# Performance work log

Measured on AMD Instinct MI355X. Metric: run time of the kernel, lower is better.

The kernel has to match this reference:

```python
import jax, jax.numpy as jnp
import numpy as np

D_K = 64
N_STEPS = 4
NEG = -1e9  # stand-in for -inf; keeps vjp NaN-free, numerically identical softmax


def setup_inputs() -> dict:
    key = jax.random.key(0)
    ks = jax.random.split(key, 12)
    B, N, D = 4, 2048, 1024
    s = 0.02
    return {
        "hidden": jax.random.normal(ks[0], (B, N, D), jnp.float32),
        "W1": jax.random.normal(ks[1], (64, D), jnp.float32) * s,
        "b1": jnp.zeros((64,), jnp.float32),
        "W2": jax.random.normal(ks[2], (28, 64), jnp.float32) * s,
        "b2": jnp.zeros((28,), jnp.float32),
        "Wq": jax.random.normal(ks[3], (D_K, 28), jnp.float32) * s,
        "Wk": jax.random.normal(ks[4], (D_K, 28), jnp.float32) * s,
        "Wc": jax.random.normal(ks[5], (1, 28), jnp.float32) * s,
        "bc": jnp.zeros((1,), jnp.float32),
        "Wv": jax.random.normal(ks[6], (D_K, D), jnp.float32) * s,
        "Wo": jax.random.normal(ks[7], (D, D_K), jnp.float32) * s,  # torch inits this to zeros; randomized for a non-trivial baseline
        "step_size": jnp.asarray(0.5, jnp.float32),
        "charge_decay": jnp.asarray(0.3, jnp.float32),
        "layer_idx": 0,
    }


def reference(hidden, W1, b1, W2, b2, Wq, Wk, Wc, bc, Wv, Wo, step_size, charge_decay, layer_idx):
    B, N, D = hidden.shape
    # features come from detached hidden in the torch code
    h_sg = jax.lax.stop_gradient(hidden)
    f = jax.nn.gelu(h_sg @ W1.T + b1, approximate=False)  # [B,N,64]
    features = jax.nn.sigmoid(f @ W2.T + b2)              # [B,N,28]
    Q = features @ Wq.T                                   # [B,N,64]
    K = features @ Wk.T                                   # [B,N,64]
    compat = jnp.einsum('bnd,bmd->bnm', Q, K) / jnp.float32(np.sqrt(D_K))
    charge = jax.nn.sigmoid(features @ Wc.T + bc)[..., 0]  # [B,N]
    causal = jnp.tril(jnp.ones((N, N), dtype=bool))
    logits = jnp.where(causal, compat, NEG)
    for _ in range(N_STEPS):
        attn = jax.nn.softmax(logits, axis=-1)            # [B,N,N]
        received = attn.sum(axis=-2)                      # [B,N]
        charge = charge * (1.0 - charge_decay * jax.nn.sigmoid(received - 1.0))
        energy = -compat * charge[:, :, None] * charge[:, None, :]
        logits = jnp.where(causal, logits - step_size * energy, NEG)
    attn = jax.nn.softmax(logits, axis=-1)
    V = hidden @ Wv.T                                     # [B,N,64]
    out = jnp.einsum('bnm,bmd->bnd', attn, V) @ Wo.T      # [B,N,D]
    return out * 0.1
```

## Files before the change

### kernel.cpp

```cpp
#include <hip/hip_runtime.h>
#include <hip/hip_bf16.h>

typedef unsigned short ushort_t;
typedef short bf16x8 __attribute__((ext_vector_type(8)));
typedef ushort_t u16x8 __attribute__((ext_vector_type(8)));
typedef ushort_t u16x4 __attribute__((ext_vector_type(4)));
typedef float f32x4 __attribute__((ext_vector_type(4)));

#define DEV static __device__ __forceinline__

DEV float bf2f(ushort_t u) { unsigned v = ((unsigned)u) << 16; float f; __builtin_memcpy(&f, &v, 4); return f; }
DEV short f2bf(float x) { __hip_bfloat16 h = __float2bfloat16(x); short s; __builtin_memcpy(&s, &h, 2); return s; }
DEV float sigm(float x) { return 1.0f / (1.0f + __expf(-x)); }

DEV bf16x8 cvt8(float4 a0, float4 a1) {
    bf16x8 t;
    t[0] = f2bf(a0.x); t[1] = f2bf(a0.y); t[2] = f2bf(a0.z); t[3] = f2bf(a0.w);
    t[4] = f2bf(a1.x); t[5] = f2bf(a1.y); t[6] = f2bf(a1.z); t[7] = f2bf(a1.w);
    return t;
}
DEV bf16x8 ld8f(const float* __restrict__ p) {
    return cvt8(*reinterpret_cast<const float4*>(p), *reinterpret_cast<const float4*>(p + 4));
}

__global__ void k_cvtW(const float* __restrict__ W1, const float* __restrict__ Wv,
                       ushort_t* __restrict__ Wcat) {
    int i = blockIdx.x * 256 + threadIdx.x;
    const float* src = (i < 8192) ? (W1 + (long)i * 8) : (Wv + (long)(i - 8192) * 8);
    const float4* p = reinterpret_cast<const float4*>(src);
    *reinterpret_cast<bf16x8*>(Wcat + (long)i * 8) = cvt8(p[0], p[1]);
}

__global__ __launch_bounds__(256) void k_fvfeat(const float* __restrict__ hidden,
        const ushort_t* __restrict__ Wcat, const float* __restrict__ b1,
        const float* __restrict__ W2, const float* __restrict__ b2,
        const float* __restrict__ Wq, const float* __restrict__ Wk,
        const float* __restrict__ Wc, const float* __restrict__ bc,
        ushort_t* __restrict__ Qb, ushort_t* __restrict__ Kb,
        ushort_t* __restrict__ VbT, float* __restrict__ charge0) {
    __shared__ float w2L[28 * 65], wqL[64 * 29], wkL[64 * 29], wcL[28], b2L[28];
    __shared__ float fLDS[16][65], featL[4][28];
    int tid = threadIdx.x;
    for (int i = tid; i < 28 * 64; i += 256) w2L[(i >> 6) * 65 + (i & 63)] = W2[i];
    for (int i = tid; i < 64 * 28; i += 256) {
        int r = i / 28, c = i - r * 28;
        wqL[r * 29 + c] = Wq[i];
        wkL[r * 29 + c] = Wk[i];
    }
    if (tid < 28) { wcL[tid] = Wc[tid]; b2L[tid] = b2[tid]; }

    int m0 = blockIdx.x * 16;
    int wave = tid >> 6, lane = tid & 63, l16 = lane & 15, quad = lane >> 4;
    int cb = (wave & 1) * 32;
    int brow_off = (wave < 2) ? 0 : 64;
    f32x4 acc[2] = {};
    const float* arow = hidden + (long)(m0 + l16) * 1024;
    const ushort_t* brow0 = Wcat + (long)(brow_off + cb + l16) * 1024;
    const ushort_t* brow1 = Wcat + (long)(brow_off + cb + 16 + l16) * 1024;
    for (int kc = 0; kc < 1024; kc += 128) {
#pragma unroll
        for (int u = 0; u < 4; u++) {
            int ko = kc + u * 32 + quad * 8;
            bf16x8 a = ld8f(arow + ko);
            bf16x8 b0 = *reinterpret_cast<const bf16x8*>(brow0 + ko);
            bf16x8 b1f = *reinterpret_cast<const bf16x8*>(brow1 + ko);
            acc[0] = __builtin_amdgcn_mfma_f32_16x16x32_bf16(a, b0, acc[0], 0, 0, 0);
            acc[1] = __builtin_amdgcn_mfma_f32_16x16x32_bf16(a, b1f, acc[1], 0, 0, 0);
        }
    }
    if (wave < 2) {
        float b1a = b1[cb + l16], b1b = b1[cb + 16 + l16];
#pragma unroll
        for (int c = 0; c < 2; c++) {
            float bv = c ? b1b : b1a;
#pragma unroll
            for (int rr = 0; rr < 4; rr++) {
                float x = acc[c][rr] + bv;
                fLDS[quad * 4 + rr][cb + c * 16 + l16] =
                    0.5f * x * (1.0f + erff(x * 0.70710678118654752f));
            }
        }
    } else {
#pragma unroll
        for (int c = 0; c < 2; c++)
#pragma unroll
            for (int rr = 0; rr < 4; rr++)
                VbT[(long)(cb + c * 16 + l16) * 8192 + (m0 + quad * 4 + rr)] =
                    (ushort_t)f2bf(acc[c][rr]);
    }
    __syncthreads();
    float bcv = bc[0];
    for (int it = 0; it < 4; it++) {
        int rowl = it * 4 + wave;
        int row = m0 + rowl;
        if (lane < 28) {
            float s = b2L[lane];
#pragma unroll
            for (int j = 0; j < 64; j++) s += fLDS[rowl][j] * w2L[lane * 65 + j];
            featL[wave][lane] = sigm(s);
        }
        __syncthreads();
        float q = 0.f, k = 0.f;
#pragma unroll
        for (int i = 0; i < 28; i++) {
            float fv = featL[wave][i];
            q += fv * wqL[lane * 29 + i];
            k += fv * wkL[lane * 29 + i];
        }
        Qb[row * 64 + lane] = (ushort_t)f2bf(q * 0.125f);
        Kb[row * 64 + lane] = (ushort_t)f2bf(k);
        if (lane == 0) {
            float c = bcv;
#pragma unroll
            for (int i = 0; i < 28; i++) c += featL[wave][i] * wcL[i];
            charge0[row] = sigm(c);
        }
        __syncthreads();
    }
}

DEV void tri_decode(int r, int& ti, int& tj) {
    int t = (int)((sqrtf(8.f * (float)r + 1.f) - 1.f) * 0.5f);
    while ((t + 1) * (t + 2) / 2 <= r) t++;
    while (t * (t + 1) / 2 > r) t--;
    ti = t;
    tj = r - t * (t + 1) / 2;
}

__global__ __launch_bounds__(256) void k_compat(const ushort_t* __restrict__ Qb,
                                                const ushort_t* __restrict__ Kb,
                                                ushort_t* __restrict__ compat) {
    int bid = blockIdx.x;
    int b = bid / 136, r = bid % 136, ti, tj;
    tri_decode(r, ti, tj);
    int wave = threadIdx.x >> 6, lane = threadIdx.x & 63;
    int l16 = lane & 15, quad = lane >> 4;
    int rbase = b * 2048 + ti * 128 + wave * 32;
    int cbase = b * 2048 + tj * 128;
    f32x4 acc[2][8] = {};
#pragma unroll
    for (int kc = 0; kc < 64; kc += 32) {
        int ko = kc + quad * 8;
        bf16x8 af[2], bf[8];
#pragma unroll
        for (int f = 0; f < 2; f++)
            af[f] = *reinterpret_cast<const bf16x8*>(Qb + (long)(rbase + f * 16 + l16) * 64 + ko);
#pragma unroll
        for (int f = 0; f < 8; f++)
            bf[f] = *reinterpret_cast<const bf16x8*>(Kb + (long)(cbase + f * 16 + l16) * 64 + ko);
#pragma unroll
        for (int i = 0; i < 2; i++)
#pragma unroll
            for (int j = 0; j < 8; j++)
                acc[i][j] = __builtin_amdgcn_mfma_f32_16x16x32_bf16(af[i], bf[j], acc[i][j], 0, 0, 0);
    }
    int colt = tj * 128;
#pragma unroll
    for (int i = 0; i < 2; i++)
#pragma unroll
        for (int j = 0; j < 8; j++)
#pragma unroll
            for (int rr = 0; rr < 4; rr++) {
                long rowg = rbase + i * 16 + quad * 4 + rr;
                int col = colt + j * 16 + l16;
                compat[rowg * 2048 + col] = (ushort_t)f2bf(acc[i][j][rr]);
            }
}

template <int T>
__global__ __launch_bounds__(256, 2) void k_strip(const ushort_t* __restrict__ compat,
        const float4* __restrict__ charges4, const float* __restrict__ stepp,
        float* __restrict__ Rpart) {
    __shared__ float chR[4][8];
    __shared__ float red[4][8], Li[8];
    int bid = blockIdx.x, tid = threadIdx.x;
    int b = bid >> 8, pi = bid & 255;
    int r0A = pi * 4, r0B = 2044 - pi * 4;
    float step = stepp[0];
    if (T > 0 && tid < 8) {
        int row = (tid < 4) ? (r0A + tid) : (r0B + tid - 4);
        float4 c4 = charges4[b * 2048 + row];
        chR[0][tid] = step * c4.x;
        if (T > 1) chR[1][tid] = step * c4.y;
        if (T > 2) chR[2][tid] = step * c4.z;
        if (T > 3) chR[3][tid] = step * c4.w;
    }
    __syncthreads();
    int w = tid >> 6, lane = tid & 63;
    int c0 = tid * 4;
    const ushort_t* base = compat + (long)(b * 2048) * 2048;

    float pA[4][4], pB0[4][4], pB1[4][4];
    float SA[4] = {}, SB[4] = {};

    {
        float cx[4] = {}, cy[4] = {}, cz[4] = {}, cw[4] = {};
        if (T > 0) {
#pragma unroll
            for (int k = 0; k < 4; k++) {
                float4 c = charges4[b * 2048 + c0 + k];
                cx[k] = c.x;
                if (T > 1) cy[k] = c.y;
                if (T > 2) cz[k] = c.z;
                if (T > 3) cw[k] = c.w;
            }
        }
#pragma unroll
        for (int rr = 0; rr < 4; rr++) {
            u16x4 v = *reinterpret_cast<const u16x4*>(base + (long)(r0A + rr) * 2048 + c0);
#pragma unroll
            for (int k = 0; k < 4; k++) {
                float sg = 1.f;
                if (T > 0) sg += chR[0][rr] * cx[k];
                if (T > 1) sg += chR[1][rr] * cy[k];
                if (T > 2) sg += chR[2][rr] * cz[k];
                if (T > 3) sg += chR[3][rr] * cw[k];
                float p = (c0 + k <= r0A + rr) ? __expf(bf2f(v[k]) * sg) : 0.f;
                pA[rr][k] = p;
                SA[rr] += p;
            }
        }
#pragma unroll
        for (int rr = 0; rr < 4; rr++) {
            u16x4 v = *reinterpret_cast<const u16x4*>(base + (long)(r0B + rr) * 2048 + c0);
#pragma unroll
            for (int k = 0; k < 4; k++) {
                float sg = 1.f;
                if (T > 0) sg += chR[0][4 + rr] * cx[k];
                if (T > 1) sg += chR[1][4 + rr] * cy[k];
                if (T > 2) sg += chR[2][4 + rr] * cz[k];
                if (T > 3) sg += chR[3][4 + rr] * cw[k];
                float p = __expf(bf2f(v[k]) * sg);
                pB0[rr][k] = p;
                SB[rr] += p;
            }
        }
    }
    {
        float cx[4] = {}, cy[4] = {}, cz[4] = {}, cw[4] = {};
        if (T > 0) {
#pragma unroll
            for (int k = 0; k < 4; k++) {
                float4 c = charges4[b * 2048 + 1024 + c0 + k];
                cx[k] = c.x;
                if (T > 1) cy[k] = c.y;
                if (T > 2) cz[k] = c.z;
                if (T > 3) cw[k] = c.w;
            }
        }
#pragma unroll
        for (int rr = 0; rr < 4; rr++) {
            u16x4 v = *reinterpret_cast<const u16x4*>(base + (long)(r0B + rr) * 2048 + 1024 + c0);
#pragma unroll
            for (int k = 0; k < 4; k++) {
                float sg = 1.f;
                if (T > 0) sg += chR[0][4 + rr] * cx[k];
                if (T > 1) sg += chR[1][4 + rr] * cy[k];
                if (T > 2) sg += chR[2][4 + rr] * cz[k];
                if (T > 3) sg += chR[3][4 + rr] * cw[k];
                float p = (1024 + c0 + k <= r0B + rr) ? __expf(bf2f(v[k]) * sg) : 0.f;
                pB1[rr][k] = p;
                SB[rr] += p;
            }
        }
    }
#pragma unroll
    for (int rr = 0; rr < 4; rr++) {
        float s = SA[rr];
        s += __shfl_xor(s, 1); s += __shfl_xor(s, 2); s += __shfl_xor(s, 4);
        s += __shfl_xor(s, 8); s += __shfl_xor(s, 16); s += __shfl_xor(s, 32);
        if (lane == 0) red[w][rr] = s;
        float t = SB[rr];
        t += __shfl_xor(t, 1); t += __shfl_xor(t, 2); t += __shfl_xor(t, 4);
        t += __shfl_xor(t, 8); t += __shfl_xor(t, 16); t += __shfl_xor(t, 32);
        if (lane == 0) red[w][4 + rr] = t;
    }
    __syncthreads();
    if (tid < 8) Li[tid] = 1.f / fmaxf(red[0][tid] + red[1][tid] + red[2][tid] + red[3][tid], 1e-30f);
    __syncthreads();
    float liA0 = Li[0], liA1 = Li[1], liA2 = Li[2], liA3 = Li[3];
    float liB0 = Li[4], liB1 = Li[5], liB2 = Li[6], liB3 = Li[7];
    float4 o0, o1;
    float* po0 = (float*)&o0;
    float* po1 = (float*)&o1;
#pragma unroll
    for (int k = 0; k < 4; k++) {
        po0[k] = pA[0][k] * liA0 + pA[1][k] * liA1 + pA[2][k] * liA2 + pA[3][k] * liA3
               + pB0[0][k] * liB0 + pB0[1][k] * liB1 + pB0[2][k] * liB2 + pB0[3][k] * liB3;
        po1[k] = pB1[0][k] * liB0 + pB1[1][k] * liB1 + pB1[2][k] * liB2 + pB1[3][k] * liB3;
    }
    *reinterpret_cast<float4*>(&Rpart[(long)bid * 2048 + c0]) = o0;
    *reinterpret_cast<float4*>(&Rpart[(long)bid * 2048 + 1024 + c0]) = o1;
}

template <int T>
__global__ __launch_bounds__(256) void k_charge(const float* __restrict__ Rpart,
        const float* __restrict__ charge0, float4* __restrict__ charges4,
        const float* __restrict__ decayp) {
    __shared__ float s8[8][33];
    int g = threadIdx.x >> 5, cl = threadIdx.x & 31;
    int m = blockIdx.x * 32 + cl;
    int b = m >> 11, col = m & 2047;
    const float* rp = Rpart + ((long)(b * 256 + g * 32) * 2048) + col;
    float s = 0.f;
#pragma unroll
    for (int i = 0; i < 32; i++) s += rp[(long)i * 2048];
    s8[g][cl] = s;
    __syncthreads();
    if (threadIdx.x < 32) {
        float t = 0.f;
#pragma unroll
        for (int gg = 0; gg < 8; gg++) t += s8[gg][threadIdx.x];
        int mm = blockIdx.x * 32 + threadIdx.x;
        float decay = decayp[0];
        float prev = (T == 1) ? charge0[mm] : ((const float*)&charges4[mm])[T - 2];
        ((float*)&charges4[mm])[T - 1] = prev * (1.f - decay * sigm(t - 1.f));
    }
}

__global__ __launch_bounds__(256, 2) void k_stripPV(const ushort_t* __restrict__ compat,
        const float4* __restrict__ charges4, const float* __restrict__ stepp,
        const ushort_t* __restrict__ VbT, ushort_t* __restrict__ Abf) {
    __shared__ float chR[4][16], red[4][16], Li[16];
    __shared__ __align__(16) ushort_t pbuf[16][1032];
    int bid = blockIdx.x, tid = threadIdx.x;
    int b = bid >> 7, pi = bid & 127;
    int r0A = pi * 8, r0B = 2040 - pi * 8;
    float step = stepp[0];
    if (tid < 16) {
        int row = (tid < 8) ? (r0A + tid) : (r0B + tid - 8);
        float4 c4 = charges4[b * 2048 + row];
        chR[0][tid] = step * c4.x; chR[1][tid] = step * c4.y;
        chR[2][tid] = step * c4.z; chR[3][tid] = step * c4.w;
    }
    __syncthreads();
    int w = tid >> 6, lane = tid & 63, l16 = lane & 15, quad = lane >> 4;
    int c0 = tid * 4;
    const ushort_t* base = compat + (long)(b * 2048) * 2048;
    float S[16];
#pragma unroll
    for (int i = 0; i < 16; i++) S[i] = 0.f;
    f32x4 acc = {};

    {
        float cx[4], cy[4], cz[4], cw[4];
#pragma unroll
        for (int k = 0; k < 4; k++) {
            float4 c = charges4[b * 2048 + c0 + k];
            cx[k] = c.x; cy[k] = c.y; cz[k] = c.z; cw[k] = c.w;
        }
#pragma unroll
        for (int i = 0; i < 16; i++) {
            int grow = (i < 8) ? (r0A + i) : (r0B + i - 8);
            u16x4 v = *reinterpret_cast<const u16x4*>(base + (long)grow * 2048 + c0);
            u16x4 pv;
#pragma unroll
            for (int k = 0; k < 4; k++) {
                float sg = 1.f + chR[0][i] * cx[k] + chR[1][i] * cy[k]
                               + chR[2][i] * cz[k] + chR[3][i] * cw[k];
                float p = __expf(bf2f(v[k]) * sg);
                if (i < 8 && (c0 + k > r0A + i)) p = 0.f;
                S[i] += p;
                pv[k] = (ushort_t)f2bf(p);
            }
            *reinterpret_cast<u16x4*>(&pbuf[i][c0]) = pv;
        }
    }
    __syncthreads();
#pragma unroll
    for (int k0 = 0; k0 < 1024; k0 += 32) {
        bf16x8 af = *reinterpret_cast<const bf16x8*>(&pbuf[l16][k0 + quad * 8]);
        bf16x8 vf = *reinterpret_cast<const bf16x8*>(
            VbT + (long)(w * 16 + l16) * 8192 + b * 2048 + k0 + quad * 8);
        acc = __builtin_amdgcn_mfma_f32_16x16x32_bf16(af, vf, acc, 0, 0, 0);
    }
    __syncthreads();
    {
        float cx[4], cy[4], cz[4], cw[4];
#pragma unroll
        for (int k = 0; k < 4; k++) {
            float4 c = charges4[b * 2048 + 1024 + c0 + k];
            cx[k] = c.x; cy[k] = c.y; cz[k] = c.z; cw[k] = c.w;
        }
        u16x4 z = {0, 0, 0, 0};
#pragma unroll
        for (int i = 0; i < 8; i++) *reinterpret_cast<u16x4*>(&pbuf[i][c0]) = z;
#pragma unroll
        for (int i = 8; i < 16; i++) {
            int grow = r0B + i - 8;
            u16x4 v = *reinterpret_cast<const u16x4*>(base + (long)grow * 2048 + 1024 + c0);
            u16x4 pv;
#pragma unroll
            for (int k = 0; k < 4; k++) {
                float sg = 1.f + chR[0][i] * cx[k] + chR[1][i] * cy[k]
                               + chR[2][i] * cz[k] + chR[3][i] * cw[k];
                float p = (1024 + c0 + k <= grow) ? __expf(bf2f(v[k]) * sg) : 0.f;
                S[i] += p;
                pv[k] = (ushort_t)f2bf(p);
            }
            *reinterpret_cast<u16x4*>(&pbuf[i][c0]) = pv;
        }
    }
    __syncthreads();
#pragma unroll
    for (int k0 = 0; k0 < 1024; k0 += 32) {
        bf16x8 af = *reinterpret_cast<const bf16x8*>(&pbuf[l16][k0 + quad * 8]);
        bf16x8 vf = *reinterpret_cast<const bf16x8*>(
            VbT + (long)(w * 16 + l16) * 8192 + b * 2048 + 1024 + k0 + quad * 8);
        acc = __builtin_amdgcn_mfma_f32_16x16x32_bf16(af, vf, acc, 0, 0, 0);
    }
#pragma unroll
    for (int i = 0; i < 16; i++) {
        float s = S[i];
        s += __shfl_xor(s, 1); s += __shfl_xor(s, 2); s += __shfl_xor(s, 4);
        s += __shfl_xor(s, 8); s += __shfl_xor(s, 16); s += __shfl_xor(s, 32);
        if (lane == 0) red[w][i] = s;
    }
    __syncthreads();
    if (tid < 16) Li[tid] = 1.f / fmaxf(red[0][tid] + red[1][tid] + red[2][tid] + red[3][tid], 1e-30f);
    __syncthreads();
#pragma unroll
    for (int rr = 0; rr < 4; rr++) {
        int row16 = quad * 4 + rr;
        int grow = (row16 < 8) ? (b * 2048 + r0A + row16) : (b * 2048 + r0B + row16 - 8);
        Abf[(long)grow * 64 + w * 16 + l16] = (ushort_t)f2bf(acc[rr] * Li[row16]);
    }
}

__global__ __launch_bounds__(256) void k_oproj(const ushort_t* __restrict__ Abf,
                                               const float* __restrict__ Wo,
                                               float* __restrict__ out) {
    int mt = blockIdx.x & 63, nt = blockIdx.x >> 6;
    int wave = threadIdx.x >> 6, lane = threadIdx.x & 63;
    int wm = wave >> 1, wn = wave & 1;
    int l16 = lane & 15, quad = lane >> 4;
    int row0 = mt * 128 + wm * 64;
    int col0 = nt * 128 + wn * 64;
    f32x4 acc[4][4] = {};
#pragma unroll
    for (int kc = 0; kc < 64; kc += 32) {
        int ko = kc + quad * 8;
        bf16x8 af[4], bfm[4];
#pragma unroll
        for (int f = 0; f < 4; f++)
            af[f] = *reinterpret_cast<const bf16x8*>(Abf + (long)(row0 + f * 16 + l16) * 64 + ko);
#pragma unroll
        for (int f = 0; f < 4; f++) bfm[f] = ld8f(Wo + (long)(col0 + f * 16 + l16) * 64 + ko);
#pragma unroll
        for (int i = 0; i < 4; i++)
#pragma unroll
            for (int j = 0; j < 4; j++)
                acc[i][j] = __builtin_amdgcn_mfma_f32_16x16x32_bf16(af[i], bfm[j], acc[i][j], 0, 0, 0);
    }
#pragma unroll
    for (int i = 0; i < 4; i++)
#pragma unroll
        for (int j = 0; j < 4; j++)
#pragma unroll
            for (int rr = 0; rr < 4; rr++) {
                long rowg = row0 + i * 16 + quad * 4 + rr;
                int colg = col0 + j * 16 + l16;
                out[rowg * 1024 + colg] = acc[i][j][rr] * 0.1f;
            }
}

extern "C" void kernel_launch(void* const* d_in, const int* in_sizes, int n_in,
                              void* d_out, int out_size, void* d_ws, size_t ws_size,
                              hipStream_t stream) {
    const float* hidden = (const float*)d_in[0];
    const float* W1 = (const float*)d_in[1];
    const float* b1 = (const float*)d_in[2];
    const float* W2 = (const float*)d_in[3];
    const float* b2 = (const float*)d_in[4];
    const float* Wq = (const float*)d_in[5];
    const float* Wk = (const float*)d_in[6];
    const float* Wc = (const float*)d_in[7];
    const float* bc = (const float*)d_in[8];
    const float* Wv = (const float*)d_in[9];
    const float* Wo = (const float*)d_in[10];
    const float* stepp = (const float*)d_in[11];
    const float* decayp = (const float*)d_in[12];

    char* ws = (char*)d_ws;
    size_t off = 0;
    auto alloc = [&](size_t bytes) {
        void* p = ws + off;
        off += (bytes + 255) & ~(size_t)255;
        return p;
    };
    ushort_t* compat = (ushort_t*)alloc(8192UL * 2048 * 2);
    ushort_t* Wcat = (ushort_t*)alloc(128UL * 1024 * 2);
    ushort_t* Qb = (ushort_t*)alloc(8192UL * 64 * 2);
    ushort_t* Kb = (ushort_t*)alloc(8192UL * 64 * 2);
    ushort_t* VbT = (ushort_t*)alloc(64UL * 8192 * 2);
    float* charge0 = (float*)alloc(8192UL * 4);
    float4* charges4 = (float4*)alloc(8192UL * 16);
    float* Rpart = (float*)alloc(1024UL * 2048 * 4);
    ushort_t* Abf = (ushort_t*)alloc(8192UL * 64 * 2);
    (void)ws_size; (void)in_sizes; (void)n_in; (void)out_size;

    k_cvtW<<<64, 256, 0, stream>>>(W1, Wv, Wcat);
    k_fvfeat<<<512, 256, 0, stream>>>(hidden, Wcat, b1, W2, b2, Wq, Wk, Wc, bc,
                                      Qb, Kb, VbT, charge0);
    k_compat<<<544, 256, 0, stream>>>(Qb, Kb, compat);

    k_strip<0><<<1024, 256, 0, stream>>>(compat, charges4, stepp, Rpart);
    k_charge<1><<<256, 256, 0, stream>>>(Rpart, charge0, charges4, decayp);
    k_strip<1><<<1024, 256, 0, stream>>>(compat, charges4, stepp, Rpart);
    k_charge<2><<<256, 256, 0, stream>>>(Rpart, charge0, charges4, decayp);
    k_strip<2><<<1024, 256, 0, stream>>>(compat, charges4, stepp, Rpart);
    k_charge<3><<<256, 256, 0, stream>>>(Rpart, charge0, charges4, decayp);
    k_strip<3><<<1024, 256, 0, stream>>>(compat, charges4, stepp, Rpart);
    k_charge<4><<<256, 256, 0, stream>>>(Rpart, charge0, charges4, decayp);

    k_stripPV<<<512, 256, 0, stream>>>(compat, charges4, stepp, VbT, Abf);
    k_oproj<<<512, 256, 0, stream>>>(Abf, Wo, (float*)d_out);
}
```

Before: 280.5 us.

## Skip fully-masked causal chunks and halve rows per block in final PV strip

In k_strip, threads whose 4-column chunk lies entirely above the causal diagonal now skip the compat loads and exp work for the A rows and the second half of B rows. k_stripPV moves from 16 rows per block to 8 (4 top, 4 mirrored bottom) with 1024 blocks and a higher occupancy hint, and applies the same masked-chunk skipping. Its MFMA A-operand maps the unused 8 of 16 rows to a zeroed pbuf row. This wastes half of the MFMA M dimension and re-reads VbT twice as often across blocks, in exchange for less masked work, more parallelism and smaller LDS use.

```diff
diff --git a/kernel.cpp b/kernel.cpp
--- a/kernel.cpp
+++ b/kernel.cpp
@@ -190,7 +190,7 @@
     int c0 = tid * 4;
     const ushort_t* base = compat + (long)(b * 2048) * 2048;
 
-    float pA[4][4], pB0[4][4], pB1[4][4];
+    float pA[4][4] = {}, pB0[4][4] = {}, pB1[4][4] = {};
     float SA[4] = {}, SB[4] = {};
 
     {
@@ -205,19 +205,21 @@
                 if (T > 3) cw[k] = c.w;
             }
         }
-#pragma unroll
-        for (int rr = 0; rr < 4; rr++) {
-            u16x4 v = *reinterpret_cast<const u16x4*>(base + (long)(r0A + rr) * 2048 + c0);
-#pragma unroll
-            for (int k = 0; k < 4; k++) {
-                float sg = 1.f;
-                if (T > 0) sg += chR[0][rr] * cx[k];
-                if (T > 1) sg += chR[1][rr] * cy[k];
-                if (T > 2) sg += chR[2][rr] * cz[k];
-                if (T > 3) sg += chR[3][rr] * cw[k];
-                float p = (c0 + k <= r0A + rr) ? __expf(bf2f(v[k]) * sg) : 0.f;
-                pA[rr][k] = p;
-                SA[rr] += p;
+        if (c0 <= r0A + 3) {
+#pragma unroll
+            for (int rr = 0; rr < 4; rr++) {
+                u16x4 v = *reinterpret_cast<const u16x4*>(base + (long)(r0A + rr) * 2048 + c0);
+#pragma unroll
+                for (int k = 0; k < 4; k++) {
+                    float sg = 1.f;
+                    if (T > 0) sg += chR[0][rr] * cx[k];
+                    if (T > 1) sg += chR[1][rr] * cy[k];
+                    if (T > 2) sg += chR[2][rr] * cz[k];
+                    if (T > 3) sg += chR[3][rr] * cw[k];
+                    float p = (c0 + k <= r0A + rr) ? __expf(bf2f(v[k]) * sg) : 0.f;
+                    pA[rr][k] = p;
+                    SA[rr] += p;
+                }
             }
         }
 #pragma unroll
@@ -236,7 +238,7 @@
             }
         }
     }
-    {
+    if (1024 + c0 <= r0B + 3) {
         float cx[4] = {}, cy[4] = {}, cz[4] = {}, cw[4] = {};
         if (T > 0) {
 #pragma unroll
@@ -318,28 +320,31 @@
     }
 }
 
-__global__ __launch_bounds__(256, 2) void k_stripPV(const ushort_t* __restrict__ compat,
+__global__ __launch_bounds__(256, 4) void k_stripPV(const ushort_t* __restrict__ compat,
         const float4* __restrict__ charges4, const float* __restrict__ stepp,
         const ushort_t* __restrict__ VbT, ushort_t* __restrict__ Abf) {
-    __shared__ float chR[4][16], red[4][16], Li[16];
-    __shared__ __align__(16) ushort_t pbuf[16][1032];
+    __shared__ float chR[4][8], red[4][8], Li[8];
+    __shared__ __align__(16) ushort_t pbuf[9][1032];
     int bid = blockIdx.x, tid = threadIdx.x;
-    int b = bid >> 7, pi = bid & 127;
-    int r0A = pi * 8, r0B = 2040 - pi * 8;
+    int b = bid >> 8, pi = bid & 255;
+    int r0A = pi * 4, r0B = 2044 - pi * 4;
     float step = stepp[0];
-    if (tid < 16) {
-        int row = (tid < 8) ? (r0A + tid) : (r0B + tid - 8);
+    if (tid < 8) {
+        int row = (tid < 4) ? (r0A + tid) : (r0B + tid - 4);
         float4 c4 = charges4[b * 2048 + row];
         chR[0][tid] = step * c4.x; chR[1][tid] = step * c4.y;
         chR[2][tid] = step * c4.z; chR[3][tid] = step * c4.w;
     }
+    u16x4 zz = {0, 0, 0, 0};
+    *reinterpret_cast<u16x4*>(&pbuf[8][tid * 4]) = zz;
     __syncthreads();
     int w = tid >> 6, lane = tid & 63, l16 = lane & 15, quad = lane >> 4;
+    int pr = (l16 < 8) ? l16 : 8;
     int c0 = tid * 4;
     const ushort_t* base = compat + (long)(b * 2048) * 2048;
-    float S[16];
-#pragma unroll
-    for (int i = 0; i < 16; i++) S[i] = 0.f;
+    float S[8];
+#pragma unroll
+    for (int i = 0; i < 8; i++) S[i] = 0.f;
     f32x4 acc = {};
 
     {
@@ -349,17 +354,34 @@
             float4 c = charges4[b * 2048 + c0 + k];
             cx[k] = c.x; cy[k] = c.y; cz[k] = c.z; cw[k] = c.w;
         }
-#pragma unroll
-        for (int i = 0; i < 16; i++) {
-            int grow = (i < 8) ? (r0A + i) : (r0B + i - 8);
-            u16x4 v = *reinterpret_cast<const u16x4*>(base + (long)grow * 2048 + c0);
+        if (c0 <= r0A + 3) {
+#pragma unroll
+            for (int i = 0; i < 4; i++) {
+                u16x4 v = *reinterpret_cast<const u16x4*>(base + (long)(r0A + i) * 2048 + c0);
+                u16x4 pv;
+#pragma unroll
+                for (int k = 0; k < 4; k++) {
+                    float sg = 1.f + chR[0][i] * cx[k] + chR[1][i] * cy[k]
+                                   + chR[2][i] * cz[k] + chR[3][i] * cw[k];
+                    float p = (c0 + k <= r0A + i) ? __expf(bf2f(v[k]) * sg) : 0.f;
+                    S[i] += p;
+                    pv[k] = (ushort_t)f2bf(p);
+                }
+                *reinterpret_cast<u16x4*>(&pbuf[i][c0]) = pv;
+            }
+        } else {
+#pragma unroll
+            for (int i = 0; i < 4; i++) *reinterpret_cast<u16x4*>(&pbuf[i][c0]) = zz;
+        }
+#pragma unroll
+        for (int i = 4; i < 8; i++) {
+            u16x4 v = *reinterpret_cast<const u16x4*>(base + (long)(r0B + i - 4) * 2048 + c0);
             u16x4 pv;
 #pragma unroll
             for (int k = 0; k < 4; k++) {
                 float sg = 1.f + chR[0][i] * cx[k] + chR[1][i] * cy[k]
                                + chR[2][i] * cz[k] + chR[3][i] * cw[k];
                 float p = __expf(bf2f(v[k]) * sg);
-                if (i < 8 && (c0 + k > r0A + i)) p = 0.f;
                 S[i] += p;
                 pv[k] = (ushort_t)f2bf(p);
             }
@@ -367,63 +389,69 @@
         }
     }
     __syncthreads();
-#pragma unroll
+#pragma unroll 4
     for (int k0 = 0; k0 < 1024; k0 += 32) {
-        bf16x8 af = *reinterpret_cast<const bf16x8*>(&pbuf[l16][k0 + quad * 8]);
+        bf16x8 af = *reinterpret_cast<const bf16x8*>(&pbuf[pr][k0 + quad * 8]);
         bf16x8 vf = *reinterpret_cast<const bf16x8*>(
             VbT + (long)(w * 16 + l16) * 8192 + b * 2048 + k0 + quad * 8);
         acc = __builtin_amdgcn_mfma_f32_16x16x32_bf16(af, vf, acc, 0, 0, 0);
     }
     __syncthreads();
     {
-        float cx[4], cy[4], cz[4], cw[4];
-#pragma unroll
-        for (int k = 0; k < 4; k++) {
-            float4 c = charges4[b * 2048 + 1024 + c0 + k];
-            cx[k] = c.x; cy[k] = c.y; cz[k] = c.z; cw[k] = c.w;
-        }
-        u16x4 z = {0, 0, 0, 0};
-#pragma unroll
-        for (int i = 0; i < 8; i++) *reinterpret_cast<u16x4*>(&pbuf[i][c0]) = z;
-#pragma unroll
-        for (int i = 8; i < 16; i++) {
-            int grow = r0B + i - 8;
-            u16x4 v = *reinterpret_cast<const u16x4*>(base + (long)grow * 2048 + 1024 + c0);
-            u16x4 pv;
+#pragma unroll
+        for (int i = 0; i < 4; i++) *reinterpret_cast<u16x4*>(&pbuf[i][c0]) = zz;
+        if (1024 + c0 <= r0B + 3) {
+            float cx[4], cy[4], cz[4], cw[4];
 #pragma unroll
             for (int k = 0; k < 4; k++) {
-                float sg = 1.f + chR[0][i] * cx[k] + chR[1][i] * cy[k]
-                               + chR[2][i] * cz[k] + chR[3][i] * cw[k];
-                float p = (1024 + c0 + k <= grow) ? __expf(bf2f(v[k]) * sg) : 0.f;
-                S[i] += p;
-                pv[k] = (ushort_t)f2bf(p);
-            }
-            *reinterpret_cast<u16x4*>(&pbuf[i][c0]) = pv;
-        }
-    }
-    __syncthreads();
-#pragma unroll
+                float4 c = charges4[b * 2048 + 1024 + c0 + k];
+                cx[k] = c.x; cy[k] = c.y; cz[k] = c.z; cw[k] = c.w;
+            }
+#pragma unroll
+            for (int i = 4; i < 8; i++) {
+                int grow = r0B + i - 4;
+                u16x4 v = *reinterpret_cast<const u16x4*>(base + (long)grow * 2048 + 1024 + c0);
+                u16x4 pv;
+#pragma unroll
+                for (int k = 0; k < 4; k++) {
+                    float sg = 1.f + chR[0][i] * cx[k] + chR[1][i] * cy[k]
+                                   + chR[2][i] * cz[k] + chR[3][i] * cw[k];
+                    float p = (1024 + c0 + k <= grow) ? __expf(bf2f(v[k]) * sg) : 0.f;
+                    S[i] += p;
+                    pv[k] = (ushort_t)f2bf(p);
+                }
+                *reinterpret_cast<u16x4*>(&pbuf[i][c0]) = pv;
+            }
+        } else {
+#pragma unroll
+            for (int i = 4; i < 8; i++) *reinterpret_cast<u16x4*>(&pbuf[i][c0]) = zz;
+        }
+    }
+    __syncthreads();
+#pragma unroll 4
     for (int k0 = 0; k0 < 1024; k0 += 32) {
-        bf16x8 af = *reinterpret_cast<const bf16x8*>(&pbuf[l16][k0 + quad * 8]);
+        bf16x8 af = *reinterpret_cast<const bf16x8*>(&pbuf[pr][k0 + quad * 8]);
         bf16x8 vf = *reinterpret_cast<const bf16x8*>(
             VbT + (long)(w * 16 + l16) * 8192 + b * 2048 + 1024 + k0 + quad * 8);
         acc = __builtin_amdgcn_mfma_f32_16x16x32_bf16(af, vf, acc, 0, 0, 0);
     }
 #pragma unroll
-    for (int i = 0; i < 16; i++) {
+    for (int i = 0; i < 8; i++) {
         float s = S[i];
         s += __shfl_xor(s, 1); s += __shfl_xor(s, 2); s += __shfl_xor(s, 4);
         s += __shfl_xor(s, 8); s += __shfl_xor(s, 16); s += __shfl_xor(s, 32);
         if (lane == 0) red[w][i] = s;
     }
     __syncthreads();
-    if (tid < 16) Li[tid] = 1.f / fmaxf(red[0][tid] + red[1][tid] + red[2][tid] + red[3][tid], 1e-30f);
-    __syncthreads();
-#pragma unroll
-    for (int rr = 0; rr < 4; rr++) {
-        int row16 = quad * 4 + rr;
-        int grow = (row16 < 8) ? (b * 2048 + r0A + row16) : (b * 2048 + r0B + row16 - 8);
-        Abf[(long)grow * 64 + w * 16 + l16] = (ushort_t)f2bf(acc[rr] * Li[row16]);
+    if (tid < 8) Li[tid] = 1.f / fmaxf(red[0][tid] + red[1][tid] + red[2][tid] + red[3][tid], 1e-30f);
+    __syncthreads();
+    if (quad < 2) {
+#pragma unroll
+        for (int rr = 0; rr < 4; rr++) {
+            int row8 = quad * 4 + rr;
+            int grow = (row8 < 4) ? (b * 2048 + r0A + row8) : (b * 2048 + r0B + row8 - 4);
+            Abf[(long)grow * 64 + w * 16 + l16] = (ushort_t)f2bf(acc[rr] * Li[row8]);
+        }
     }
 }
 
@@ -513,6 +541,6 @@
     k_strip<3><<<1024, 256, 0, stream>>>(compat, charges4, stepp, Rpart);
     k_charge<4><<<256, 256, 0, stream>>>(Rpart, charge0, charges4, decayp);
 
-    k_stripPV<<<512, 256, 0, stream>>>(compat, charges4, stepp, VbT, Abf);
+    k_stripPV<<<1024, 256, 0, stream>>>(compat, charges4, stepp, VbT, Abf);
     k_oproj<<<512, 256, 0, stream>>>(Abf, Wo, (float*)d_out);
 }
```

Measured after the change: 261.7 us. 1.07x faster.
